# Kernel optimization log

Measured on AMD Instinct MI355X. Metric: run time of the kernel, lower is better.

The kernel has to match this reference:

```python
import jax, jax.numpy as jnp
import numpy as np

N_NODES = 100000
N_EDGES = 1600000
IN_F, HID, N_COLORS = 128, 128, 10


def setup_inputs() -> dict:
    key = jax.random.key(0)
    k1, k2, k3, k4 = jax.random.split(key, 4)
    x = jax.random.normal(k1, (N_NODES, IN_F), dtype=jnp.float32)
    edge_index = jax.random.randint(k2, (2, N_EDGES), 0, N_NODES, dtype=jnp.int64)
    # Glorot-ish init for weights
    W1 = jax.random.normal(k3, (IN_F, HID), dtype=jnp.float32) / np.sqrt(IN_F)
    b1 = jnp.zeros((HID,), dtype=jnp.float32)
    W2 = jax.random.normal(k4, (HID, N_COLORS), dtype=jnp.float32) / np.sqrt(HID)
    b2 = jnp.zeros((N_COLORS,), dtype=jnp.float32)
    return {"x": x, "edge_index": edge_index, "W1": W1, "b1": b1, "W2": W2, "b2": b2}


def _gcn_norm(edge_index, num_nodes):
    # Add self-loops, compute symmetric normalization D^-1/2 (A+I) D^-1/2
    loops = jnp.arange(num_nodes, dtype=edge_index.dtype)
    src = jnp.concatenate([edge_index[0], loops])
    dst = jnp.concatenate([edge_index[1], loops])
    deg = jax.ops.segment_sum(jnp.ones_like(dst, dtype=jnp.float32), dst,
                              num_segments=num_nodes)
    deg_isqrt = jax.lax.rsqrt(deg)  # deg >= 1 due to self-loops
    norm = deg_isqrt[src] * deg_isqrt[dst]  # [E + N]
    return src, dst, norm


def _gcn_conv(h, src, dst, norm, num_nodes, W, b):
    # Linear transform first (PyG GCNConv), then gather-scale-scatter aggregate
    h = h @ W                                   # [N, out]
    msg = h[src] * norm[:, None]                # [E + N, out] gather
    out = jax.ops.segment_sum(msg, dst, num_segments=num_nodes)  # scatter-add
    return out + b


def reference(x, edge_index, W1, b1, W2, b2):
    n = x.shape[0]
    src, dst, norm = _gcn_norm(edge_index, n)
    h = _gcn_conv(x, src, dst, norm, n, W1, b1)
    h = jax.nn.relu(h)
    # dropout is identity in eval mode
    h = _gcn_conv(h, src, dst, norm, n, W2, b2)
    return jax.nn.softmax(h, axis=1)
```

## Files before the change

kernel.cpp:

```cpp
#include <hip/hip_runtime.h>
#include <hip/hip_fp16.h>

#define IN_F 128
#define HID  128
#define NC   10
#define H2P  16
#define NPB  128
#define NBMAX 784
#define BCAP 2560
#define EPB  4096

typedef _Float16 f16x8 __attribute__((ext_vector_type(8)));
typedef float f32x4 __attribute__((ext_vector_type(4)));
typedef int int4a __attribute__((ext_vector_type(4), aligned(4)));

__device__ inline __half2 shfl_xor_h2(__half2 v, int mask) {
    int i = __shfl_xor(*reinterpret_cast<int*>(&v), mask, 64);
    return *reinterpret_cast<__half2*>(&i);
}

__global__ __launch_bounds__(1024) void k_bin(const int* __restrict__ src,
                                              const int* __restrict__ dst,
                                              int* __restrict__ bcnt,
                                              unsigned int* __restrict__ binned,
                                              const float* __restrict__ W1,
                                              __half* __restrict__ WT,
                                              int E, int nbin) {
    __shared__ int hist[NBMAX];
    __shared__ int base[NBMAX];
    __shared__ int lcur[NBMAX];
    const int tid = threadIdx.x;

    if (blockIdx.x == 0) {
        for (int i = tid; i < IN_F * HID; i += 1024) {
            int k = i >> 7, n = i & 127;
            WT[n * IN_F + k] = __float2half(W1[k * HID + n]);
        }
    }

    for (int b = tid; b < nbin; b += 1024) { hist[b] = 0; lcur[b] = 0; }
    __syncthreads();

    const int e0 = blockIdx.x * EPB + tid;
    int d[4];
    #pragma unroll
    for (int u = 0; u < 4; u++) {
        int e = e0 + u * 1024;
        d[u] = (e < E) ? dst[e] : -1;
        if (d[u] >= 0) atomicAdd(&hist[d[u] >> 7], 1);
    }
    __syncthreads();
    for (int b = tid; b < nbin; b += 1024) {
        int h = hist[b];
        base[b] = h ? atomicAdd(&bcnt[b], h) : 0;
    }
    __syncthreads();
    #pragma unroll
    for (int u = 0; u < 4; u++) {
        int e = e0 + u * 1024;
        if (e < E) {
            int dd = d[u];
            int b = dd >> 7;
            int s = src[e];
            int o = base[b] + atomicAdd(&lcur[b], 1);
            if (o < BCAP)
                binned[(size_t)b * BCAP + o] = ((unsigned)(dd & 127) << 17) | (unsigned)s;
        }
    }
}

__global__ __launch_bounds__(256) void k_place2(const int* __restrict__ bcnt,
                                                const unsigned int* __restrict__ binned,
                                                int* __restrict__ rowptr,
                                                float* __restrict__ dis,
                                                int* __restrict__ csr,
                                                int N, int E, int nbin) {
    __shared__ int h[NPB];
    __shared__ int lb[NPB];
    __shared__ int cur[NPB];
    __shared__ int red[256];
    const int b = blockIdx.x;
    const int tid = threadIdx.x;

    int partial = 0;
    for (int i = tid; i < b; i += 256) partial += bcnt[i];
    red[tid] = partial;
    if (tid < NPB) h[tid] = 0;
    __syncthreads();
    #pragma unroll
    for (int off = 128; off > 0; off >>= 1) {
        if (tid < off) red[tid] += red[tid + off];
        __syncthreads();
    }
    const int rb = red[0];

    const int m = min(bcnt[b], BCAP);
    const unsigned int* p = binned + (size_t)b * BCAP;
    for (int i = tid; i < m; i += 256) atomicAdd(&h[p[i] >> 17], 1);
    __syncthreads();
    if (tid < NPB) lb[tid] = h[tid];
    __syncthreads();
    #pragma unroll
    for (int off = 1; off < NPB; off <<= 1) {
        int t = (tid < NPB && tid >= off) ? lb[tid - off] : 0;
        __syncthreads();
        if (tid < NPB) lb[tid] += t;
        __syncthreads();
    }
    if (tid < NPB) {
        int ex = lb[tid] - h[tid];
        int node = b * NPB + tid;
        if (node < N) {
            rowptr[node] = rb + ex;
            dis[node] = rsqrtf(1.0f + (float)h[tid]);
        }
        lb[tid] = ex;
        cur[tid] = 0;
    }
    if (b == nbin - 1 && tid == 0) rowptr[N] = E;
    __syncthreads();
    for (int i = tid; i < m; i += 256) {
        unsigned v = p[i];
        int dl = v >> 17;
        int r = atomicAdd(&cur[dl], 1);
        csr[rb + lb[dl] + r] = (int)(v & 0x1FFFF);
    }
}

__global__ __launch_bounds__(256) void k_gemm1(const float* __restrict__ X,
                                               const __half* __restrict__ WT,
                                               const float* __restrict__ dis,
                                               __half* __restrict__ outh) {
    __shared__ _Float16 sX[32 * IN_F];
    __shared__ _Float16 sW[128 * IN_F];
    const int tid = threadIdx.x;
    const int row0 = blockIdx.x * 32;

    {
        int n = tid >> 1, part = tid & 1;
        const f16x8* src = (const f16x8*)(WT + n * IN_F + part * 64);
        f16x8* dst = (f16x8*)(sW + n * IN_F + part * 64);
        #pragma unroll
        for (int c = 0; c < 8; c++) dst[c] = src[c];
    }
    {
        int r = tid >> 3;
        int k0 = (tid & 7) * 16;
        const float* sp = X + (size_t)(row0 + r) * IN_F + k0;
        float4 f0 = *(const float4*)(sp);
        float4 f1 = *(const float4*)(sp + 4);
        float4 f2 = *(const float4*)(sp + 8);
        float4 f3 = *(const float4*)(sp + 12);
        f16x8 h0, h1;
        h0[0] = (_Float16)f0.x; h0[1] = (_Float16)f0.y;
        h0[2] = (_Float16)f0.z; h0[3] = (_Float16)f0.w;
        h0[4] = (_Float16)f1.x; h0[5] = (_Float16)f1.y;
        h0[6] = (_Float16)f1.z; h0[7] = (_Float16)f1.w;
        h1[0] = (_Float16)f2.x; h1[1] = (_Float16)f2.y;
        h1[2] = (_Float16)f2.z; h1[3] = (_Float16)f2.w;
        h1[4] = (_Float16)f3.x; h1[5] = (_Float16)f3.y;
        h1[6] = (_Float16)f3.z; h1[7] = (_Float16)f3.w;
        *(f16x8*)(sX + r * IN_F + k0) = h0;
        *(f16x8*)(sX + r * IN_F + k0 + 8) = h1;
    }
    __syncthreads();

    const int wave = tid >> 6;
    const int lane = tid & 63;
    const int quad = lane >> 4;
    const int l16 = lane & 15;
    const int nbase = wave * 32;

    f32x4 acc00 = {0,0,0,0}, acc01 = {0,0,0,0}, acc10 = {0,0,0,0}, acc11 = {0,0,0,0};

    #pragma unroll
    for (int kc = 0; kc < 4; kc++) {
        const int koff = kc * 32 + quad * 8;
        f16x8 a0 = *(const f16x8*)(sX + l16 * IN_F + koff);
        f16x8 a1 = *(const f16x8*)(sX + (16 + l16) * IN_F + koff);
        f16x8 b0 = *(const f16x8*)(sW + (nbase + l16) * IN_F + koff);
        f16x8 b1 = *(const f16x8*)(sW + (nbase + 16 + l16) * IN_F + koff);
        acc00 = __builtin_amdgcn_mfma_f32_16x16x32_f16(a0, b0, acc00, 0, 0, 0);
        acc01 = __builtin_amdgcn_mfma_f32_16x16x32_f16(a0, b1, acc01, 0, 0, 0);
        acc10 = __builtin_amdgcn_mfma_f32_16x16x32_f16(a1, b0, acc10, 0, 0, 0);
        acc11 = __builtin_amdgcn_mfma_f32_16x16x32_f16(a1, b1, acc11, 0, 0, 0);
    }

    #pragma unroll
    for (int r = 0; r < 4; r++) {
        {
            int row = row0 + quad * 4 + r;
            float d = dis[row];
            __half* o = outh + (size_t)row * HID + nbase + l16;
            o[0]  = __float2half(acc00[r] * d);
            o[16] = __float2half(acc01[r] * d);
        }
        {
            int row = row0 + 16 + quad * 4 + r;
            float d = dis[row];
            __half* o = outh + (size_t)row * HID + nbase + l16;
            o[0]  = __float2half(acc10[r] * d);
            o[16] = __float2half(acc11[r] * d);
        }
    }
}

__global__ __launch_bounds__(256) void k_agg1(const __half* __restrict__ hsh,
                                              const int* __restrict__ rowptr,
                                              const int* __restrict__ csr,
                                              const float* __restrict__ dis,
                                              const float* __restrict__ b1,
                                              const float* __restrict__ W2,
                                              __half* __restrict__ h2h,
                                              int N, int E) {
    __shared__ float sWT[NC][IN_F];
    for (int i = threadIdx.x; i < NC * IN_F; i += 256)
        sWT[i >> 7][i & 127] = W2[(i & 127) * NC + (i >> 7)];
    __syncthreads();

    const int node = blockIdx.x * 4 + (threadIdx.x >> 6);
    if (node >= N) return;
    const int lane = threadIdx.x & 63;
    const int g   = lane >> 4;
    const int l16 = lane & 15;
    const int f0  = l16 * 8;

    const int beg = rowptr[node], end = rowptr[node + 1];
    const __half2 hz = __half2half2(__float2half(0.0f));
    const __half2 ho = __half2half2(__float2half(1.0f));
    const unsigned nclamp = (unsigned)(N - 1);

    __half2 acc2[4] = {hz, hz, hz, hz};
    if (g == 0) {
        float4 r = *(const float4*)(hsh + (size_t)node * HID + f0);
        const __half2* hh = (const __half2*)&r;
        acc2[0] = hh[0]; acc2[1] = hh[1]; acc2[2] = hh[2]; acc2[3] = hh[3];
    }

    for (int j0 = beg + 4 * g; j0 < end; j0 += 16) {
        int bj = min(j0, E - 4);
        int off = j0 - bj;
        int rem = end - j0;
        int4a cv = *(const int4a*)(csr + bj);
        unsigned s0 = min((unsigned)cv[0], nclamp);
        unsigned s1 = min((unsigned)cv[1], nclamp);
        unsigned s2 = min((unsigned)cv[2], nclamp);
        unsigned s3 = min((unsigned)cv[3], nclamp);
        __half2 w0 = ((unsigned)(0 - off) < (unsigned)rem) ? ho : hz;
        __half2 w1 = ((unsigned)(1 - off) < (unsigned)rem) ? ho : hz;
        __half2 w2 = ((unsigned)(2 - off) < (unsigned)rem) ? ho : hz;
        __half2 w3 = ((unsigned)(3 - off) < (unsigned)rem) ? ho : hz;
        float4 r0 = *(const float4*)(hsh + (size_t)s0 * HID + f0);
        float4 r1 = *(const float4*)(hsh + (size_t)s1 * HID + f0);
        float4 r2 = *(const float4*)(hsh + (size_t)s2 * HID + f0);
        float4 r3 = *(const float4*)(hsh + (size_t)s3 * HID + f0);
        const __half2* h0 = (const __half2*)&r0;
        const __half2* h1 = (const __half2*)&r1;
        const __half2* h2 = (const __half2*)&r2;
        const __half2* h3 = (const __half2*)&r3;
        #pragma unroll
        for (int i = 0; i < 4; i++) {
            acc2[i] = __hfma2(w0, h0[i], acc2[i]);
            acc2[i] = __hfma2(w1, h1[i], acc2[i]);
            acc2[i] = __hfma2(w2, h2[i], acc2[i]);
            acc2[i] = __hfma2(w3, h3[i], acc2[i]);
        }
    }

    #pragma unroll
    for (int i = 0; i < 4; i++) {
        acc2[i] = __hadd2(acc2[i], shfl_xor_h2(acc2[i], 16));
        acc2[i] = __hadd2(acc2[i], shfl_xor_h2(acc2[i], 32));
    }
    float acc[8];
    #pragma unroll
    for (int i = 0; i < 4; i++) {
        float2 t = __half22float2(acc2[i]);
        acc[2 * i] = t.x; acc[2 * i + 1] = t.y;
    }

    const float d = dis[node];
    float4 ba = *(const float4*)(b1 + f0);
    float4 bb = *(const float4*)(b1 + f0 + 4);
    float h[8];
    h[0] = fmaxf(fmaf(d, acc[0], ba.x), 0.0f);
    h[1] = fmaxf(fmaf(d, acc[1], ba.y), 0.0f);
    h[2] = fmaxf(fmaf(d, acc[2], ba.z), 0.0f);
    h[3] = fmaxf(fmaf(d, acc[3], ba.w), 0.0f);
    h[4] = fmaxf(fmaf(d, acc[4], bb.x), 0.0f);
    h[5] = fmaxf(fmaf(d, acc[5], bb.y), 0.0f);
    h[6] = fmaxf(fmaf(d, acc[6], bb.z), 0.0f);
    h[7] = fmaxf(fmaf(d, acc[7], bb.w), 0.0f);

    const int cb = (g == 0) ? 0 : (g == 1) ? 3 : (g == 2) ? 6 : 8;
    const int nc = (g < 2) ? 3 : 2;
    float p[3];
    #pragma unroll
    for (int ci = 0; ci < 3; ci++) {
        if (ci < nc) {
            int c = cb + ci;
            float4 wa = *(const float4*)&sWT[c][f0];
            float4 wb = *(const float4*)&sWT[c][f0 + 4];
            float t = fmaf(h[0], wa.x, fmaf(h[1], wa.y, fmaf(h[2], wa.z, h[3] * wa.w)));
            t = fmaf(h[4], wb.x, fmaf(h[5], wb.y, fmaf(h[6], wb.z, fmaf(h[7], wb.w, t))));
            #pragma unroll
            for (int off = 1; off < 16; off <<= 1) t += __shfl_xor(t, off, 64);
            p[ci] = t;
        }
    }
    if (l16 == 0) {
        __half* o = h2h + (size_t)node * H2P + cb;
        for (int ci = 0; ci < nc; ci++) o[ci] = __float2half(d * p[ci]);
    }
}

__global__ __launch_bounds__(256) void k_agg2(const __half* __restrict__ h2h,
                                              const int* __restrict__ rowptr,
                                              const int* __restrict__ csr,
                                              const float* __restrict__ dis,
                                              const float* __restrict__ b2,
                                              float* __restrict__ out,
                                              int N, int E) {
    int t = blockIdx.x * 256 + threadIdx.x;
    int node = t >> 1;
    int q = t & 1;
    if (node >= N) return;
    const int base = q * 8;
    const __half2 hz = __half2half2(__float2half(0.0f));
    const __half2 ho = __half2half2(__float2half(1.0f));
    const unsigned nclamp = (unsigned)(N - 1);

    __half2 a2[4];
    {
        float4 r = *(const float4*)(h2h + (size_t)node * H2P + base);
        const __half2* hh = (const __half2*)&r;
        a2[0] = hh[0]; a2[1] = hh[1]; a2[2] = hh[2]; a2[3] = hh[3];
    }
    const int beg = rowptr[node], end = rowptr[node + 1];
    for (int j0 = beg; j0 < end; j0 += 4) {
        int bj = min(j0, E - 4);
        int off = j0 - bj;
        int rem = end - j0;
        int4a cv = *(const int4a*)(csr + bj);
        unsigned s0 = min((unsigned)cv[0], nclamp);
        unsigned s1 = min((unsigned)cv[1], nclamp);
        unsigned s2 = min((unsigned)cv[2], nclamp);
        unsigned s3 = min((unsigned)cv[3], nclamp);
        __half2 w0 = ((unsigned)(0 - off) < (unsigned)rem) ? ho : hz;
        __half2 w1 = ((unsigned)(1 - off) < (unsigned)rem) ? ho : hz;
        __half2 w2 = ((unsigned)(2 - off) < (unsigned)rem) ? ho : hz;
        __half2 w3 = ((unsigned)(3 - off) < (unsigned)rem) ? ho : hz;
        float4 r0 = *(const float4*)(h2h + (size_t)s0 * H2P + base);
        float4 r1 = *(const float4*)(h2h + (size_t)s1 * H2P + base);
        float4 r2 = *(const float4*)(h2h + (size_t)s2 * H2P + base);
        float4 r3 = *(const float4*)(h2h + (size_t)s3 * H2P + base);
        const __half2* h0 = (const __half2*)&r0;
        const __half2* h1 = (const __half2*)&r1;
        const __half2* h2 = (const __half2*)&r2;
        const __half2* h3 = (const __half2*)&r3;
        #pragma unroll
        for (int i = 0; i < 4; i++) {
            a2[i] = __hfma2(w0, h0[i], a2[i]);
            a2[i] = __hfma2(w1, h1[i], a2[i]);
            a2[i] = __hfma2(w2, h2[i], a2[i]);
            a2[i] = __hfma2(w3, h3[i], a2[i]);
        }
    }

    float a[8];
    #pragma unroll
    for (int i = 0; i < 4; i++) {
        float2 tt = __half22float2(a2[i]);
        a[2 * i] = tt.x; a[2 * i + 1] = tt.y;
    }

    const float d = dis[node];
    float vv[8];
    #pragma unroll
    for (int i = 0; i < 8; i++) {
        int f = base + i;
        vv[i] = (f < NC) ? fmaf(d, a[i], b2[f]) : -1e30f;
    }
    float m = vv[0];
    #pragma unroll
    for (int i = 1; i < 8; i++) m = fmaxf(m, vv[i]);
    m = fmaxf(m, __shfl_xor(m, 1, 64));
    float e[8];
    float s = 0.0f;
    #pragma unroll
    for (int i = 0; i < 8; i++) { e[i] = (base + i < NC) ? expf(vv[i] - m) : 0.0f; s += e[i]; }
    s += __shfl_xor(s, 1, 64);
    float inv = 1.0f / s;

    float* o = out + (size_t)node * NC;
    if (q == 0) {
        *(float2*)(o + 0) = make_float2(e[0] * inv, e[1] * inv);
        *(float2*)(o + 2) = make_float2(e[2] * inv, e[3] * inv);
        *(float2*)(o + 4) = make_float2(e[4] * inv, e[5] * inv);
        *(float2*)(o + 6) = make_float2(e[6] * inv, e[7] * inv);
    } else {
        *(float2*)(o + 8) = make_float2(e[0] * inv, e[1] * inv);
    }
}

extern "C" void kernel_launch(void* const* d_in, const int* in_sizes, int n_in,
                              void* d_out, int out_size, void* d_ws, size_t ws_size,
                              hipStream_t stream) {
    const float* x  = (const float*)d_in[0];
    const int*   ei = (const int*)d_in[1];
    const float* W1 = (const float*)d_in[2];
    const float* b1 = (const float*)d_in[3];
    const float* W2 = (const float*)d_in[4];
    const float* b2 = (const float*)d_in[5];
    float* out = (float*)d_out;

    const int N = in_sizes[0] / IN_F;
    const int E = in_sizes[1] / 2;
    const int* esrc = ei;
    const int* edst = ei + E;
    const int nbin = (N + NPB - 1) / NPB;

    char* ws = (char*)d_ws;
    int*    rowptr  = (int*)(ws);
    float*  dis     = (float*)(ws + 0x80000);
    int*    bcnt    = (int*)(ws + 0x100000);
    __half* WT      = (__half*)(ws + 0x110000);
    unsigned int* binned = (unsigned int*)(ws + 0x140000);
    int*    csr     = (int*)(ws + 0x940000);
    __half* hsh     = (__half*)(ws + 0x1040000);
    __half* h2h     = (__half*)(ws + 0x2A00000);

    hipMemsetAsync(bcnt, 0, (size_t)nbin * sizeof(int), stream);

    k_bin   <<<(E + EPB - 1) / EPB, 1024, 0, stream>>>(esrc, edst, bcnt, binned, W1, WT, E, nbin);
    k_place2<<<nbin, 256, 0, stream>>>(bcnt, binned, rowptr, dis, csr, N, E, nbin);
    k_gemm1 <<<N / 32, 256, 0, stream>>>(x, WT, dis, hsh);
    k_agg1  <<<(N + 3) / 4, 256, 0, stream>>>(hsh, rowptr, csr, dis, b1, W2, h2h, N, E);
    k_agg2  <<<(int)(((size_t)N * 2 + 255) / 256), 256, 0, stream>>>(h2h, rowptr, csr, dis, b2, out, N, E);
}
```

Before: 250.8 us.

## Fuse CSR build and first GEMM into one cooperative persistent kernel

Replaces the memset, binning, placement and GEMM1 kernels with a single cooperative kernel that uses grid-wide syncs between phases. Degree is now counted with global atomics per node so dis is ready before placement, which lets CSR placement and GEMM1 tiles run concurrently in one work loop. The aim is to cut launch overhead and tail idle time between the small kernels. In exchange it adds per-edge global atomics and grid.sync costs, and the grid size is capped by occupancy.

```diff
diff --git a/kernel.cpp b/kernel.cpp
--- a/kernel.cpp
+++ b/kernel.cpp
@@ -1,5 +1,8 @@
 #include <hip/hip_runtime.h>
 #include <hip/hip_fp16.h>
+#include <hip/hip_cooperative_groups.h>
+
+namespace cg = cooperative_groups;
 
 #define IN_F 128
 #define HID  128
@@ -8,7 +11,7 @@
 #define NPB  128
 #define NBMAX 784
 #define BCAP 2560
-#define EPB  4096
+#define EPB2 4096
 
 typedef _Float16 f16x8 __attribute__((ext_vector_type(8)));
 typedef float f32x4 __attribute__((ext_vector_type(4)));
@@ -19,188 +22,196 @@
     return *reinterpret_cast<__half2*>(&i);
 }
 
-__global__ __launch_bounds__(1024) void k_bin(const int* __restrict__ src,
-                                              const int* __restrict__ dst,
-                                              int* __restrict__ bcnt,
-                                              unsigned int* __restrict__ binned,
-                                              const float* __restrict__ W1,
-                                              __half* __restrict__ WT,
-                                              int E, int nbin) {
-    __shared__ int hist[NBMAX];
-    __shared__ int base[NBMAX];
-    __shared__ int lcur[NBMAX];
+__global__ __launch_bounds__(256) void k_build(const int* __restrict__ src,
+                                               const int* __restrict__ dst,
+                                               int* __restrict__ bcnt,
+                                               unsigned int* __restrict__ binned,
+                                               const float* __restrict__ X,
+                                               const float* __restrict__ W1,
+                                               __half* __restrict__ WT,
+                                               int* __restrict__ rowptr,
+                                               float* __restrict__ dis,
+                                               int* __restrict__ cnt,
+                                               int* __restrict__ csr,
+                                               __half* __restrict__ hsh,
+                                               int N, int E, int nbin,
+                                               int nbb, int ngb) {
+    __shared__ __align__(16) char smem[40960];
+    cg::grid_group grid = cg::this_grid();
     const int tid = threadIdx.x;
-
-    if (blockIdx.x == 0) {
-        for (int i = tid; i < IN_F * HID; i += 1024) {
-            int k = i >> 7, n = i & 127;
-            WT[n * IN_F + k] = __float2half(W1[k * HID + n]);
+    const int gsize = gridDim.x * 256;
+    const int gtid = blockIdx.x * 256 + tid;
+
+    for (int i = gtid; i < nbin; i += gsize) bcnt[i] = 0;
+    for (int i = gtid; i < N; i += gsize) cnt[i] = 0;
+    for (int i = gtid; i < IN_F * HID; i += gsize) {
+        int k = i >> 7, n = i & 127;
+        WT[n * IN_F + k] = __float2half(W1[i]);
+    }
+    grid.sync();
+
+    {
+        int* hist = (int*)smem;
+        int* base = hist + NBMAX;
+        int* lcur = base + NBMAX;
+        for (int vb = blockIdx.x; vb < nbb; vb += gridDim.x) {
+            for (int b = tid; b < nbin; b += 256) { hist[b] = 0; lcur[b] = 0; }
+            __syncthreads();
+            const int e0 = vb * EPB2 + tid;
+            int d[16];
+            #pragma unroll
+            for (int u = 0; u < 16; u++) {
+                int e = e0 + u * 256;
+                d[u] = (e < E) ? dst[e] : -1;
+                if (d[u] >= 0) {
+                    atomicAdd(&hist[d[u] >> 7], 1);
+                    atomicAdd(&cnt[d[u]], 1);
+                }
+            }
+            __syncthreads();
+            for (int b = tid; b < nbin; b += 256) {
+                int h = hist[b];
+                base[b] = h ? atomicAdd(&bcnt[b], h) : 0;
+            }
+            __syncthreads();
+            #pragma unroll
+            for (int u = 0; u < 16; u++) {
+                int e = e0 + u * 256;
+                if (e < E) {
+                    int dd = d[u];
+                    int b = dd >> 7;
+                    int s = src[e];
+                    int o = base[b] + atomicAdd(&lcur[b], 1);
+                    if (o < BCAP)
+                        binned[(size_t)b * BCAP + o] = ((unsigned)(dd & 127) << 17) | (unsigned)s;
+                }
+            }
+            __syncthreads();
         }
     }
-
-    for (int b = tid; b < nbin; b += 1024) { hist[b] = 0; lcur[b] = 0; }
-    __syncthreads();
-
-    const int e0 = blockIdx.x * EPB + tid;
-    int d[4];
-    #pragma unroll
-    for (int u = 0; u < 4; u++) {
-        int e = e0 + u * 1024;
-        d[u] = (e < E) ? dst[e] : -1;
-        if (d[u] >= 0) atomicAdd(&hist[d[u] >> 7], 1);
-    }
-    __syncthreads();
-    for (int b = tid; b < nbin; b += 1024) {
-        int h = hist[b];
-        base[b] = h ? atomicAdd(&bcnt[b], h) : 0;
-    }
-    __syncthreads();
-    #pragma unroll
-    for (int u = 0; u < 4; u++) {
-        int e = e0 + u * 1024;
-        if (e < E) {
-            int dd = d[u];
-            int b = dd >> 7;
-            int s = src[e];
-            int o = base[b] + atomicAdd(&lcur[b], 1);
-            if (o < BCAP)
-                binned[(size_t)b * BCAP + o] = ((unsigned)(dd & 127) << 17) | (unsigned)s;
-        }
-    }
-}
-
-__global__ __launch_bounds__(256) void k_place2(const int* __restrict__ bcnt,
-                                                const unsigned int* __restrict__ binned,
-                                                int* __restrict__ rowptr,
-                                                float* __restrict__ dis,
-                                                int* __restrict__ csr,
-                                                int N, int E, int nbin) {
-    __shared__ int h[NPB];
-    __shared__ int lb[NPB];
-    __shared__ int cur[NPB];
-    __shared__ int red[256];
-    const int b = blockIdx.x;
-    const int tid = threadIdx.x;
-
-    int partial = 0;
-    for (int i = tid; i < b; i += 256) partial += bcnt[i];
-    red[tid] = partial;
-    if (tid < NPB) h[tid] = 0;
-    __syncthreads();
-    #pragma unroll
-    for (int off = 128; off > 0; off >>= 1) {
-        if (tid < off) red[tid] += red[tid + off];
-        __syncthreads();
-    }
-    const int rb = red[0];
-
-    const int m = min(bcnt[b], BCAP);
-    const unsigned int* p = binned + (size_t)b * BCAP;
-    for (int i = tid; i < m; i += 256) atomicAdd(&h[p[i] >> 17], 1);
-    __syncthreads();
-    if (tid < NPB) lb[tid] = h[tid];
-    __syncthreads();
-    #pragma unroll
-    for (int off = 1; off < NPB; off <<= 1) {
-        int t = (tid < NPB && tid >= off) ? lb[tid - off] : 0;
-        __syncthreads();
-        if (tid < NPB) lb[tid] += t;
-        __syncthreads();
-    }
-    if (tid < NPB) {
-        int ex = lb[tid] - h[tid];
-        int node = b * NPB + tid;
-        if (node < N) {
-            rowptr[node] = rb + ex;
-            dis[node] = rsqrtf(1.0f + (float)h[tid]);
-        }
-        lb[tid] = ex;
-        cur[tid] = 0;
-    }
-    if (b == nbin - 1 && tid == 0) rowptr[N] = E;
-    __syncthreads();
-    for (int i = tid; i < m; i += 256) {
-        unsigned v = p[i];
-        int dl = v >> 17;
-        int r = atomicAdd(&cur[dl], 1);
-        csr[rb + lb[dl] + r] = (int)(v & 0x1FFFF);
-    }
-}
-
-__global__ __launch_bounds__(256) void k_gemm1(const float* __restrict__ X,
-                                               const __half* __restrict__ WT,
-                                               const float* __restrict__ dis,
-                                               __half* __restrict__ outh) {
-    __shared__ _Float16 sX[32 * IN_F];
-    __shared__ _Float16 sW[128 * IN_F];
-    const int tid = threadIdx.x;
-    const int row0 = blockIdx.x * 32;
-
+    grid.sync();
+
+    for (int i = gtid; i < N; i += gsize) dis[i] = rsqrtf(1.0f + (float)cnt[i]);
+    grid.sync();
+
+    _Float16* sX = (_Float16*)smem;
+    _Float16* sW = (_Float16*)(smem + 8192);
     {
         int n = tid >> 1, part = tid & 1;
-        const f16x8* src = (const f16x8*)(WT + n * IN_F + part * 64);
-        f16x8* dst = (f16x8*)(sW + n * IN_F + part * 64);
+        const f16x8* s = (const f16x8*)(WT + n * IN_F + part * 64);
+        f16x8* dws = (f16x8*)(sW + n * IN_F + part * 64);
         #pragma unroll
-        for (int c = 0; c < 8; c++) dst[c] = src[c];
-    }
-    {
-        int r = tid >> 3;
-        int k0 = (tid & 7) * 16;
-        const float* sp = X + (size_t)(row0 + r) * IN_F + k0;
-        float4 f0 = *(const float4*)(sp);
-        float4 f1 = *(const float4*)(sp + 4);
-        float4 f2 = *(const float4*)(sp + 8);
-        float4 f3 = *(const float4*)(sp + 12);
-        f16x8 h0, h1;
-        h0[0] = (_Float16)f0.x; h0[1] = (_Float16)f0.y;
-        h0[2] = (_Float16)f0.z; h0[3] = (_Float16)f0.w;
-        h0[4] = (_Float16)f1.x; h0[5] = (_Float16)f1.y;
-        h0[6] = (_Float16)f1.z; h0[7] = (_Float16)f1.w;
-        h1[0] = (_Float16)f2.x; h1[1] = (_Float16)f2.y;
-        h1[2] = (_Float16)f2.z; h1[3] = (_Float16)f2.w;
-        h1[4] = (_Float16)f3.x; h1[5] = (_Float16)f3.y;
-        h1[6] = (_Float16)f3.z; h1[7] = (_Float16)f3.w;
-        *(f16x8*)(sX + r * IN_F + k0) = h0;
-        *(f16x8*)(sX + r * IN_F + k0 + 8) = h1;
-    }
-    __syncthreads();
-
-    const int wave = tid >> 6;
-    const int lane = tid & 63;
-    const int quad = lane >> 4;
-    const int l16 = lane & 15;
-    const int nbase = wave * 32;
-
-    f32x4 acc00 = {0,0,0,0}, acc01 = {0,0,0,0}, acc10 = {0,0,0,0}, acc11 = {0,0,0,0};
-
-    #pragma unroll
-    for (int kc = 0; kc < 4; kc++) {
-        const int koff = kc * 32 + quad * 8;
-        f16x8 a0 = *(const f16x8*)(sX + l16 * IN_F + koff);
-        f16x8 a1 = *(const f16x8*)(sX + (16 + l16) * IN_F + koff);
-        f16x8 b0 = *(const f16x8*)(sW + (nbase + l16) * IN_F + koff);
-        f16x8 b1 = *(const f16x8*)(sW + (nbase + 16 + l16) * IN_F + koff);
-        acc00 = __builtin_amdgcn_mfma_f32_16x16x32_f16(a0, b0, acc00, 0, 0, 0);
-        acc01 = __builtin_amdgcn_mfma_f32_16x16x32_f16(a0, b1, acc01, 0, 0, 0);
-        acc10 = __builtin_amdgcn_mfma_f32_16x16x32_f16(a1, b0, acc10, 0, 0, 0);
-        acc11 = __builtin_amdgcn_mfma_f32_16x16x32_f16(a1, b1, acc11, 0, 0, 0);
-    }
-
-    #pragma unroll
-    for (int r = 0; r < 4; r++) {
-        {
-            int row = row0 + quad * 4 + r;
-            float d = dis[row];
-            __half* o = outh + (size_t)row * HID + nbase + l16;
-            o[0]  = __float2half(acc00[r] * d);
-            o[16] = __float2half(acc01[r] * d);
-        }
-        {
-            int row = row0 + 16 + quad * 4 + r;
-            float d = dis[row];
-            __half* o = outh + (size_t)row * HID + nbase + l16;
-            o[0]  = __float2half(acc10[r] * d);
-            o[16] = __float2half(acc11[r] * d);
+        for (int c = 0; c < 8; c++) dws[c] = s[c];
+    }
+
+    const int tot = nbin + ngb;
+    for (int vb = blockIdx.x; vb < tot; vb += gridDim.x) {
+        __syncthreads();
+        if (vb < nbin) {
+            int* h   = (int*)smem;
+            int* lb  = h + NPB;
+            int* cur = lb + NPB;
+            int* red = cur + NPB;
+            const int b = vb;
+            int partial = 0;
+            for (int i = tid; i < b; i += 256) partial += bcnt[i];
+            red[tid] = partial;
+            if (tid < NPB) h[tid] = 0;
+            __syncthreads();
+            #pragma unroll
+            for (int off = 128; off > 0; off >>= 1) {
+                if (tid < off) red[tid] += red[tid + off];
+                __syncthreads();
+            }
+            const int rb = red[0];
+            const int m = min(bcnt[b], BCAP);
+            const unsigned int* p = binned + (size_t)b * BCAP;
+            for (int i = tid; i < m; i += 256) atomicAdd(&h[p[i] >> 17], 1);
+            __syncthreads();
+            if (tid < NPB) lb[tid] = h[tid];
+            __syncthreads();
+            #pragma unroll
+            for (int off = 1; off < NPB; off <<= 1) {
+                int t = (tid < NPB && tid >= off) ? lb[tid - off] : 0;
+                __syncthreads();
+                if (tid < NPB) lb[tid] += t;
+                __syncthreads();
+            }
+            if (tid < NPB) {
+                int ex = lb[tid] - h[tid];
+                int node = b * NPB + tid;
+                if (node < N) rowptr[node] = rb + ex;
+                lb[tid] = ex;
+                cur[tid] = 0;
+            }
+            if (b == nbin - 1 && tid == 0) rowptr[N] = E;
+            __syncthreads();
+            for (int i = tid; i < m; i += 256) {
+                unsigned v = p[i];
+                int dl = v >> 17;
+                int r = atomicAdd(&cur[dl], 1);
+                csr[rb + lb[dl] + r] = (int)(v & 0x1FFFF);
+            }
+        } else {
+            const int row0 = (vb - nbin) * 32;
+            {
+                int r = tid >> 3;
+                int k0 = (tid & 7) * 16;
+                const float* sp = X + (size_t)(row0 + r) * IN_F + k0;
+                float4 f0 = *(const float4*)(sp);
+                float4 f1 = *(const float4*)(sp + 4);
+                float4 f2 = *(const float4*)(sp + 8);
+                float4 f3 = *(const float4*)(sp + 12);
+                f16x8 h0, h1;
+                h0[0] = (_Float16)f0.x; h0[1] = (_Float16)f0.y;
+                h0[2] = (_Float16)f0.z; h0[3] = (_Float16)f0.w;
+                h0[4] = (_Float16)f1.x; h0[5] = (_Float16)f1.y;
+                h0[6] = (_Float16)f1.z; h0[7] = (_Float16)f1.w;
+                h1[0] = (_Float16)f2.x; h1[1] = (_Float16)f2.y;
+                h1[2] = (_Float16)f2.z; h1[3] = (_Float16)f2.w;
+                h1[4] = (_Float16)f3.x; h1[5] = (_Float16)f3.y;
+                h1[6] = (_Float16)f3.z; h1[7] = (_Float16)f3.w;
+                *(f16x8*)(sX + r * IN_F + k0) = h0;
+                *(f16x8*)(sX + r * IN_F + k0 + 8) = h1;
+            }
+            __syncthreads();
+
+            const int wave = tid >> 6;
+            const int lane = tid & 63;
+            const int quad = lane >> 4;
+            const int l16 = lane & 15;
+            const int nbase = wave * 32;
+
+            f32x4 acc00 = {0,0,0,0}, acc01 = {0,0,0,0}, acc10 = {0,0,0,0}, acc11 = {0,0,0,0};
+            #pragma unroll
+            for (int kc = 0; kc < 4; kc++) {
+                const int koff = kc * 32 + quad * 8;
+                f16x8 a0 = *(const f16x8*)(sX + l16 * IN_F + koff);
+                f16x8 a1 = *(const f16x8*)(sX + (16 + l16) * IN_F + koff);
+                f16x8 b0 = *(const f16x8*)(sW + (nbase + l16) * IN_F + koff);
+                f16x8 b1 = *(const f16x8*)(sW + (nbase + 16 + l16) * IN_F + koff);
+                acc00 = __builtin_amdgcn_mfma_f32_16x16x32_f16(a0, b0, acc00, 0, 0, 0);
+                acc01 = __builtin_amdgcn_mfma_f32_16x16x32_f16(a0, b1, acc01, 0, 0, 0);
+                acc10 = __builtin_amdgcn_mfma_f32_16x16x32_f16(a1, b0, acc10, 0, 0, 0);
+                acc11 = __builtin_amdgcn_mfma_f32_16x16x32_f16(a1, b1, acc11, 0, 0, 0);
+            }
+            #pragma unroll
+            for (int r = 0; r < 4; r++) {
+                {
+                    int row = row0 + quad * 4 + r;
+                    float dv = dis[row];
+                    __half* o = hsh + (size_t)row * HID + nbase + l16;
+                    o[0]  = __float2half(acc00[r] * dv);
+                    o[16] = __float2half(acc01[r] * dv);
+                }
+                {
+                    int row = row0 + 16 + quad * 4 + r;
+                    float dv = dis[row];
+                    __half* o = hsh + (size_t)row * HID + nbase + l16;
+                    o[0]  = __float2half(acc10[r] * dv);
+                    o[16] = __float2half(acc11[r] * dv);
+                }
+            }
         }
     }
 }
@@ -414,27 +425,37 @@
     const float* b2 = (const float*)d_in[5];
     float* out = (float*)d_out;
 
-    const int N = in_sizes[0] / IN_F;
-    const int E = in_sizes[1] / 2;
+    int N = in_sizes[0] / IN_F;
+    int E = in_sizes[1] / 2;
     const int* esrc = ei;
     const int* edst = ei + E;
-    const int nbin = (N + NPB - 1) / NPB;
+    int nbin = (N + NPB - 1) / NPB;
+    int nbb  = (E + EPB2 - 1) / EPB2;
+    int ngb  = N / 32;
 
     char* ws = (char*)d_ws;
     int*    rowptr  = (int*)(ws);
     float*  dis     = (float*)(ws + 0x80000);
     int*    bcnt    = (int*)(ws + 0x100000);
     __half* WT      = (__half*)(ws + 0x110000);
-    unsigned int* binned = (unsigned int*)(ws + 0x140000);
-    int*    csr     = (int*)(ws + 0x940000);
+    int*    cnt     = (int*)(ws + 0x120000);
+    unsigned int* binned = (unsigned int*)(ws + 0x1A0000);
+    int*    csr     = (int*)(ws + 0x960000);
     __half* hsh     = (__half*)(ws + 0x1040000);
     __half* h2h     = (__half*)(ws + 0x2A00000);
 
-    hipMemsetAsync(bcnt, 0, (size_t)nbin * sizeof(int), stream);
-
-    k_bin   <<<(E + EPB - 1) / EPB, 1024, 0, stream>>>(esrc, edst, bcnt, binned, W1, WT, E, nbin);
-    k_place2<<<nbin, 256, 0, stream>>>(bcnt, binned, rowptr, dis, csr, N, E, nbin);
-    k_gemm1 <<<N / 32, 256, 0, stream>>>(x, WT, dis, hsh);
-    k_agg1  <<<(N + 3) / 4, 256, 0, stream>>>(hsh, rowptr, csr, dis, b1, W2, h2h, N, E);
-    k_agg2  <<<(int)(((size_t)N * 2 + 255) / 256), 256, 0, stream>>>(h2h, rowptr, csr, dis, b2, out, N, E);
+    int maxb = 0;
+    hipOccupancyMaxActiveBlocksPerMultiprocessor(&maxb, k_build, 256, 0);
+    if (maxb < 1) maxb = 1;
+    if (maxb > 8) maxb = 8;
+    int grid = maxb * 256;
+
+    void* args[] = { (void*)&esrc, (void*)&edst, (void*)&bcnt, (void*)&binned,
+                     (void*)&x, (void*)&W1, (void*)&WT, (void*)&rowptr,
+                     (void*)&dis, (void*)&cnt, (void*)&csr, (void*)&hsh,
+                     (void*)&N, (void*)&E, (void*)&nbin, (void*)&nbb, (void*)&ngb };
+    hipLaunchCooperativeKernel((void*)k_build, dim3(grid), dim3(256), args, 0, stream);
+
+    k_agg1<<<(N + 3) / 4, 256, 0, stream>>>(hsh, rowptr, csr, dis, b1, W2, h2h, N, E);
+    k_agg2<<<(int)(((size_t)N * 2 + 255) / 256), 256, 0, stream>>>(h2h, rowptr, csr, dis, b2, out, N, E);
 }
```

Result: slower. 465.6 us (+85.7%).
